# Kernel tuning notes

Hardware: AMD Instinct MI355X
Metric: run time of the kernel (lower is better)

The kernel has to match this reference:

```python
import jax, jax.numpy as jnp
import numpy as np

C, H, V, N, T = 256, 256, 10000, 8, 256


def _residual_mlp(x, w1, b1, w2, b2, w3, b3):
    # ResidualLayerOld: relu(lin2(relu(lin1(x)))) + x, then final Linear
    h = jax.nn.relu(x @ w1 + b1)
    h = jax.nn.relu(h @ w2 + b2) + x
    return h @ w3 + b3


def setup_inputs() -> dict:
    key = jax.random.key(0)
    ks = jax.random.split(key, 16)
    p = lambda k, shape: jax.random.normal(k, shape, jnp.float32) * 0.02
    return dict(
        text=jax.random.randint(ks[0], (N, T), 0, V),
        mask=jnp.ones((N, T), dtype=bool),
        lengths=jnp.full((N,), T - 1, dtype=jnp.int32),  # full-length sequences
        start_emb=jax.random.normal(ks[1], (C, H), jnp.float32),
        state_emb=jax.random.normal(ks[2], (C, H), jnp.float32),
        preterminal_emb=jax.random.normal(ks[3], (C, H), jnp.float32),
        start_w1=p(ks[4], (H, H)), start_b1=jnp.zeros((H,), jnp.float32),
        start_w2=p(ks[5], (H, H)), start_b2=jnp.zeros((H,), jnp.float32),
        start_w3=p(ks[6], (H, 1)), start_b3=jnp.zeros((1,), jnp.float32),
        trans_w1=p(ks[7], (H, H)), trans_b1=jnp.zeros((H,), jnp.float32),
        trans_w2=p(ks[8], (H, H)), trans_b2=jnp.zeros((H,), jnp.float32),
        trans_w3=p(ks[9], (H, C)), trans_b3=jnp.zeros((C,), jnp.float32),
        term_w1=p(ks[10], (H, H)), term_b1=jnp.zeros((H,), jnp.float32),
        term_w2=p(ks[11], (H, H)), term_b2=jnp.zeros((H,), jnp.float32),
        term_w3=p(ks[12], (H, V)), term_b3=jnp.zeros((V,), jnp.float32),
    )


def _score(text, mask, lengths,
           start_emb, state_emb, preterminal_emb,
           start_w1, start_b1, start_w2, start_b2, start_w3, start_b3,
           trans_w1, trans_b1, trans_w2, trans_b2, trans_w3, trans_b3,
           term_w1, term_b1, term_w2, term_b2, term_w3, term_b3):
    n, t = text.shape
    c = state_emb.shape[0]
    # start / transition / emission distributions (dropout_type == 'none')
    init = jax.nn.log_softmax(
        _residual_mlp(start_emb, start_w1, start_b1, start_w2, start_b2, start_w3, start_b3)[:, 0], -1)  # [C]
    trans = jax.nn.log_softmax(
        _residual_mlp(state_emb, trans_w1, trans_b1, trans_w2, trans_b2, trans_w3, trans_b3), -1)  # [C,C]
    log_em = jax.nn.log_softmax(
        _residual_mlp(preterminal_emb, term_w1, term_b1, term_w2, term_b2, term_w3, term_b3), -1)  # [C,V]
    obs = log_em.T[text]  # [N,T,C], log p(x_t | z=c)
    # torch_struct LinearChain.hmm edge potentials: phi[n,t,c_next,c_prev]
    phi = trans[None, None] + obs[:, 1:, :, None]  # [N,T-1,C,C]
    phi = phi.at[:, 0].add(init[None, None, :] + obs[:, 0][:, None, :])
    phi_t = jnp.swapaxes(phi, 0, 1)  # [T-1,N,C,C]

    def fwd_step(alpha, p):
        new = jax.nn.logsumexp(p + alpha[:, None, :], axis=-1)  # reduce over c_prev
        return new, new

    _, alphas = jax.lax.scan(fwd_step, jnp.zeros((n, c), phi.dtype), phi_t)  # [T-1,N,C]

    def bwd_step(beta, p):
        new = jax.nn.logsumexp(p + beta[:, :, None], axis=1)  # reduce over c_next
        return new, beta

    _, betas = jax.lax.scan(bwd_step, jnp.zeros((n, c), phi.dtype), phi_t, reverse=True)  # [T-1,N,C]

    alpha_prev = jnp.concatenate([jnp.zeros((1, n, c), phi.dtype), alphas[:-1]], 0)
    log_Z = jax.nn.logsumexp(alphas[-1], -1)  # [N]
    # edge posteriors
    log_m = alpha_prev[:, :, None, :] + phi_t + betas[:, :, :, None] - log_Z[None, :, None, None]
    marginals = jnp.swapaxes(jnp.exp(log_m), 0, 1)  # [N,T-1,C,C]

    evidence = jax.nn.logsumexp(alphas[lengths - 1, jnp.arange(n)], -1).sum()
    elbo = jnp.where(mask[:, 1:, None, None],
                     jax.lax.stop_gradient(marginals) * phi,
                     0.0).sum()
    return elbo, evidence


def reference(text, mask, lengths,
              start_emb, state_emb, preterminal_emb,
              start_w1, start_b1, start_w2, start_b2, start_w3, start_b3,
              trans_w1, trans_b1, trans_w2, trans_b2, trans_w3, trans_b3,
              term_w1, term_b1, term_w2, term_b2, term_w3, term_b3):
    elbo, evidence = _score(text, mask, lengths,
                            start_emb, state_emb, preterminal_emb,
                            start_w1, start_b1, start_w2, start_b2, start_w3, start_b3,
                            trans_w1, trans_b1, trans_w2, trans_b2, trans_w3, trans_b3,
                            term_w1, term_b1, term_w2, term_b2, term_w3, term_b3)
    return elbo, evidence
```

## Files before the change

kernel.cpp:

```cpp
#include <hip/hip_runtime.h>
#include <hip/hip_bf16.h>

#define C_ 256
#define H_ 256
#define V_ 10000
#define N_ 8
#define T_ 256
#define TM1_ 255
#define NB_ ((V_ + 31) / 32)

typedef _Float16 h2_t __attribute__((ext_vector_type(2)));
typedef _Float16 h4_t __attribute__((ext_vector_type(4)));
typedef _Float16 h8_t __attribute__((ext_vector_type(8)));
typedef float f4v __attribute__((ext_vector_type(4)));

__device__ __forceinline__ void bar_lgkm() {
  asm volatile("s_waitcnt lgkmcnt(0)\ns_barrier" ::: "memory");
}

__device__ __forceinline__ float wave_red_max(float v) {
#define DPP_MAX(ctrl) { int iv_ = __float_as_int(v); \
  int r_ = __builtin_amdgcn_update_dpp(iv_, iv_, ctrl, 0xF, 0xF, false); \
  v = fmaxf(v, __int_as_float(r_)); }
  DPP_MAX(0x111) DPP_MAX(0x112) DPP_MAX(0x114) DPP_MAX(0x118)
  DPP_MAX(0x142) DPP_MAX(0x143)
#undef DPP_MAX
  return __int_as_float(__builtin_amdgcn_readlane(__float_as_int(v), 63));
}
__device__ __forceinline__ float wave_red_sum(float v) {
#define DPP_ADD(ctrl) { \
  int r_ = __builtin_amdgcn_update_dpp(0, __float_as_int(v), ctrl, 0xF, 0xF, true); \
  v += __int_as_float(r_); }
  DPP_ADD(0x111) DPP_ADD(0x112) DPP_ADD(0x114) DPP_ADD(0x118)
  DPP_ADD(0x142) DPP_ADD(0x143)
#undef DPP_ADD
  return __int_as_float(__builtin_amdgcn_readlane(__float_as_int(v), 63));
}

__device__ __forceinline__ float block_allmax(float v, float* red) {
  v = wave_red_max(v);
  if ((threadIdx.x & 63) == 0) red[threadIdx.x >> 6] = v;
  __syncthreads();
  v = fmaxf(fmaxf(red[0], red[1]), fmaxf(red[2], red[3]));
  __syncthreads();
  return v;
}
__device__ __forceinline__ float block_allsum(float v, float* red) {
  v = wave_red_sum(v);
  if ((threadIdx.x & 63) == 0) red[threadIdx.x >> 6] = v;
  __syncthreads();
  v = (red[0] + red[1]) + (red[2] + red[3]);
  __syncthreads();
  return v;
}

__device__ __forceinline__ void mlp4(
    const float* __restrict__ emb,
    const float* __restrict__ w1, const float* __restrict__ b1,
    const float* __restrict__ w2, const float* __restrict__ b2,
    int r0, float (&e_s)[4][C_], float (&h_s)[4][C_], float (&h2_s)[4][C_]) {
  const int tid = threadIdx.x;
#pragma unroll
  for (int rr = 0; rr < 4; ++rr)
    e_s[rr][tid] = emb[(r0 + rr) * H_ + tid];
  __syncthreads();
  float bb = b1[tid];
  float a0 = bb, a1 = bb, a2 = bb, a3 = bb;
  for (int k4 = 0; k4 < H_ / 4; ++k4) {
    float4 e0 = ((const float4*)e_s[0])[k4];
    float4 e1 = ((const float4*)e_s[1])[k4];
    float4 e2 = ((const float4*)e_s[2])[k4];
    float4 e3 = ((const float4*)e_s[3])[k4];
    const float* wp = w1 + (k4 * 4) * H_ + tid;
    float wa = wp[0], wb = wp[H_], wc = wp[2 * H_], wd = wp[3 * H_];
    a0 = fmaf(e0.x, wa, a0); a0 = fmaf(e0.y, wb, a0);
    a0 = fmaf(e0.z, wc, a0); a0 = fmaf(e0.w, wd, a0);
    a1 = fmaf(e1.x, wa, a1); a1 = fmaf(e1.y, wb, a1);
    a1 = fmaf(e1.z, wc, a1); a1 = fmaf(e1.w, wd, a1);
    a2 = fmaf(e2.x, wa, a2); a2 = fmaf(e2.y, wb, a2);
    a2 = fmaf(e2.z, wc, a2); a2 = fmaf(e2.w, wd, a2);
    a3 = fmaf(e3.x, wa, a3); a3 = fmaf(e3.y, wb, a3);
    a3 = fmaf(e3.z, wc, a3); a3 = fmaf(e3.w, wd, a3);
  }
  h_s[0][tid] = fmaxf(a0, 0.f);
  h_s[1][tid] = fmaxf(a1, 0.f);
  h_s[2][tid] = fmaxf(a2, 0.f);
  h_s[3][tid] = fmaxf(a3, 0.f);
  __syncthreads();
  bb = b2[tid];
  a0 = bb; a1 = bb; a2 = bb; a3 = bb;
  for (int k4 = 0; k4 < H_ / 4; ++k4) {
    float4 e0 = ((const float4*)h_s[0])[k4];
    float4 e1 = ((const float4*)h_s[1])[k4];
    float4 e2 = ((const float4*)h_s[2])[k4];
    float4 e3 = ((const float4*)h_s[3])[k4];
    const float* wp = w2 + (k4 * 4) * H_ + tid;
    float wa = wp[0], wb = wp[H_], wc = wp[2 * H_], wd = wp[3 * H_];
    a0 = fmaf(e0.x, wa, a0); a0 = fmaf(e0.y, wb, a0);
    a0 = fmaf(e0.z, wc, a0); a0 = fmaf(e0.w, wd, a0);
    a1 = fmaf(e1.x, wa, a1); a1 = fmaf(e1.y, wb, a1);
    a1 = fmaf(e1.z, wc, a1); a1 = fmaf(e1.w, wd, a1);
    a2 = fmaf(e2.x, wa, a2); a2 = fmaf(e2.y, wb, a2);
    a2 = fmaf(e2.z, wc, a2); a2 = fmaf(e2.w, wd, a2);
    a3 = fmaf(e3.x, wa, a3); a3 = fmaf(e3.y, wb, a3);
    a3 = fmaf(e3.z, wc, a3); a3 = fmaf(e3.w, wd, a3);
  }
  h2_s[0][tid] = fmaxf(a0, 0.f) + e_s[0][tid];
  h2_s[1][tid] = fmaxf(a1, 0.f) + e_s[1][tid];
  h2_s[2][tid] = fmaxf(a2, 0.f) + e_s[2][tid];
  h2_s[3][tid] = fmaxf(a3, 0.f) + e_s[3][tid];
  __syncthreads();
}

__global__ __launch_bounds__(256) void k_start(
    const float* __restrict__ emb, const float* __restrict__ w1,
    const float* __restrict__ b1, const float* __restrict__ w2,
    const float* __restrict__ b2, const float* __restrict__ w3,
    const float* __restrict__ b3, float* __restrict__ slogit) {
  __shared__ __align__(16) float e_s[4][C_], h_s[4][C_], h2_s[4][C_];
  __shared__ float red[4];
  const int r0 = blockIdx.x * 4;
  const int tid = threadIdx.x;
  mlp4(emb, w1, b1, w2, b2, r0, e_s, h_s, h2_s);
  float w3v = w3[tid];
  float s0 = block_allsum(h2_s[0][tid] * w3v, red);
  float s1 = block_allsum(h2_s[1][tid] * w3v, red);
  float s2 = block_allsum(h2_s[2][tid] * w3v, red);
  float s3 = block_allsum(h2_s[3][tid] * w3v, red);
  if (tid == 0) {
    float bb = b3[0];
    slogit[r0 + 0] = s0 + bb;
    slogit[r0 + 1] = s1 + bb;
    slogit[r0 + 2] = s2 + bb;
    slogit[r0 + 3] = s3 + bb;
  }
}

__global__ void k_init(const float* __restrict__ slogit, float* __restrict__ initv) {
  __shared__ float red[4];
  const int tid = threadIdx.x;
  float x = slogit[tid];
  float m = block_allmax(x, red);
  float se = block_allsum(__expf(x - m), red);
  initv[tid] = x - m - __logf(se);
}

__global__ __launch_bounds__(256) void k_trans(
    const float* __restrict__ emb, const float* __restrict__ w1,
    const float* __restrict__ b1, const float* __restrict__ w2,
    const float* __restrict__ b2, const float* __restrict__ w3,
    const float* __restrict__ b3, float* __restrict__ Pf,
    float* __restrict__ PLf, float* __restrict__ PTf,
    _Float16* __restrict__ P_h, _Float16* __restrict__ PT_h) {
  __shared__ __align__(16) float e_s[4][C_], h_s[4][C_], h2_s[4][C_];
  __shared__ float red[4];
  const int r0 = blockIdx.x * 4;
  const int tid = threadIdx.x;
  mlp4(emb, w1, b1, w2, b2, r0, e_s, h_s, h2_s);
  float lb = b3[tid];
  float l0 = lb, l1 = lb, l2 = lb, l3 = lb;
  for (int k4 = 0; k4 < H_ / 4; ++k4) {
    float4 e0 = ((const float4*)h2_s[0])[k4];
    float4 e1 = ((const float4*)h2_s[1])[k4];
    float4 e2 = ((const float4*)h2_s[2])[k4];
    float4 e3 = ((const float4*)h2_s[3])[k4];
    const float* wp = w3 + (k4 * 4) * C_ + tid;
    float wa = wp[0], wb = wp[C_], wc = wp[2 * C_], wd = wp[3 * C_];
    l0 = fmaf(e0.x, wa, l0); l0 = fmaf(e0.y, wb, l0);
    l0 = fmaf(e0.z, wc, l0); l0 = fmaf(e0.w, wd, l0);
    l1 = fmaf(e1.x, wa, l1); l1 = fmaf(e1.y, wb, l1);
    l1 = fmaf(e1.z, wc, l1); l1 = fmaf(e1.w, wd, l1);
    l2 = fmaf(e2.x, wa, l2); l2 = fmaf(e2.y, wb, l2);
    l2 = fmaf(e2.z, wc, l2); l2 = fmaf(e2.w, wd, l2);
    l3 = fmaf(e3.x, wa, l3); l3 = fmaf(e3.y, wb, l3);
    l3 = fmaf(e3.z, wc, l3); l3 = fmaf(e3.w, wd, l3);
  }
  float lg[4] = {l0, l1, l2, l3};
#pragma unroll
  for (int rr = 0; rr < 4; ++rr) {
    float m = block_allmax(lg[rr], red);
    float e = __expf(lg[rr] - m);
    float se = block_allsum(e, red);
    float p = e / se;
    float tv = lg[rr] - m - __logf(se);
    const int r = r0 + rr;
    Pf[r * C_ + tid] = p;
    PLf[r * C_ + tid] = p * tv;
    PTf[tid * C_ + r] = p;
    P_h[r * C_ + tid] = (_Float16)p;
    PT_h[tid * C_ + r] = (_Float16)p;
  }
}

__global__ __launch_bounds__(256) void k_term_mlp(
    const float* __restrict__ emb, const float* __restrict__ w1,
    const float* __restrict__ b1, const float* __restrict__ w2,
    const float* __restrict__ b2, float* __restrict__ H2,
    float* __restrict__ H2T) {
  __shared__ __align__(16) float e_s[4][C_], h_s[4][C_], h2_s[4][C_];
  const int r0 = blockIdx.x * 4;
  const int tid = threadIdx.x;
  mlp4(emb, w1, b1, w2, b2, r0, e_s, h_s, h2_s);
#pragma unroll
  for (int rr = 0; rr < 4; ++rr) {
    const int r = r0 + rr;
    float v = h2_s[rr][tid];
    H2[r * H_ + tid] = v;
    H2T[tid * C_ + r] = v;
  }
}

__global__ __launch_bounds__(256) void k_term_stats(
    const float* __restrict__ H2, const float* __restrict__ w3,
    const float* __restrict__ b3, float* __restrict__ partm,
    float* __restrict__ parts) {
  __shared__ __align__(16) float w3_s[H_][32];
  __shared__ float b3_s[32];
  const int v0 = blockIdx.x * 32;
  const int tid = threadIdx.x;
  const int ncols = min(32, V_ - v0);
  for (int idx = tid; idx < H_ * 32; idx += 256) {
    int k = idx >> 5, c = idx & 31;
    w3_s[k][c] = (c < ncols) ? w3[k * V_ + v0 + c] : 0.f;
  }
  if (tid < 32) b3_s[tid] = (tid < ncols) ? b3[v0 + tid] : 0.f;
  __syncthreads();
  float acc[32];
#pragma unroll
  for (int c = 0; c < 32; ++c) acc[c] = 0.f;
  const float4* hq = (const float4*)(H2 + tid * H_);
  for (int k4 = 0; k4 < H_ / 4; ++k4) {
    float4 h = hq[k4];
    float hk[4];
    *(float4*)hk = h;
#pragma unroll
    for (int kk = 0; kk < 4; ++kk) {
      float hv = hk[kk];
      const int k = k4 * 4 + kk;
      const float4* wq = (const float4*)(&w3_s[k][0]);
#pragma unroll
      for (int c4 = 0; c4 < 8; ++c4) {
        float4 w = wq[c4];
        acc[c4 * 4 + 0] = fmaf(hv, w.x, acc[c4 * 4 + 0]);
        acc[c4 * 4 + 1] = fmaf(hv, w.y, acc[c4 * 4 + 1]);
        acc[c4 * 4 + 2] = fmaf(hv, w.z, acc[c4 * 4 + 2]);
        acc[c4 * 4 + 3] = fmaf(hv, w.w, acc[c4 * 4 + 3]);
      }
    }
  }
  float m = -1e30f;
#pragma unroll
  for (int c = 0; c < 32; ++c) {
    acc[c] += b3_s[c];
    if (c < ncols) m = fmaxf(m, acc[c]);
  }
  float se = 0.f;
#pragma unroll
  for (int c = 0; c < 32; ++c)
    if (c < ncols) se += __expf(acc[c] - m);
  partm[blockIdx.x * C_ + tid] = m;
  parts[blockIdx.x * C_ + tid] = se;
}

__global__ void k_denom(const float* __restrict__ partm,
                        const float* __restrict__ parts,
                        float* __restrict__ denom) {
  const int r = threadIdx.x;
  float m = -1e30f;
  for (int b = 0; b < NB_; ++b) m = fmaxf(m, partm[b * C_ + r]);
  float s = 0.f;
  for (int b = 0; b < NB_; ++b)
    s += parts[b * C_ + r] * __expf(partm[b * C_ + r] - m);
  denom[r] = m + __logf(s);
}

__global__ __launch_bounds__(256) void k_obs2(
    const int* __restrict__ text, const float* __restrict__ H2T,
    const float* __restrict__ w3, const float* __restrict__ b3,
    const float* __restrict__ denom, float* __restrict__ EOBS,
    float* __restrict__ Karr) {
  __shared__ __align__(16) float w_s[H_][8];
  __shared__ float redm[4][8];
  const int c = threadIdx.x;
  const int wid = c >> 6;
  const int lane = c & 63;
  const int base = blockIdx.x * 8;
  int tok[8];
#pragma unroll
  for (int i = 0; i < 8; ++i) tok[i] = text[base + i];
  float wtmp[8];
#pragma unroll
  for (int i = 0; i < 8; ++i) wtmp[i] = w3[c * V_ + tok[i]];
  float b3t[8];
#pragma unroll
  for (int i = 0; i < 8; ++i) b3t[i] = b3[tok[i]];
#pragma unroll
  for (int i = 0; i < 8; ++i) w_s[c][i] = wtmp[i];
  __syncthreads();
  float acc[8];
#pragma unroll
  for (int i = 0; i < 8; ++i) acc[i] = 0.f;
  for (int k4 = 0; k4 < H_ / 4; ++k4) {
    float hv[4];
#pragma unroll
    for (int kk = 0; kk < 4; ++kk) hv[kk] = H2T[(k4 * 4 + kk) * C_ + c];
#pragma unroll
    for (int kk = 0; kk < 4; ++kk) {
      const float4* wq = (const float4*)(&w_s[k4 * 4 + kk][0]);
      float4 wa = wq[0], wb = wq[1];
      acc[0] = fmaf(hv[kk], wa.x, acc[0]);
      acc[1] = fmaf(hv[kk], wa.y, acc[1]);
      acc[2] = fmaf(hv[kk], wa.z, acc[2]);
      acc[3] = fmaf(hv[kk], wa.w, acc[3]);
      acc[4] = fmaf(hv[kk], wb.x, acc[4]);
      acc[5] = fmaf(hv[kk], wb.y, acc[5]);
      acc[6] = fmaf(hv[kk], wb.z, acc[6]);
      acc[7] = fmaf(hv[kk], wb.w, acc[7]);
    }
  }
  float dn = denom[c];
  float obsv[8];
#pragma unroll
  for (int i = 0; i < 8; ++i) obsv[i] = acc[i] + b3t[i] - dn;
#pragma unroll
  for (int i = 0; i < 8; ++i) {
    float wm = wave_red_max(obsv[i]);
    if (lane == 0) redm[wid][i] = wm;
  }
  __syncthreads();
#pragma unroll
  for (int i = 0; i < 8; ++i) {
    float Ki = fmaxf(fmaxf(redm[0][i], redm[1][i]),
                     fmaxf(redm[2][i], redm[3][i]));
    EOBS[(base + i) * C_ + c] = __expf(obsv[i] - Ki);
    if (c == 0) Karr[base + i] = Ki;
  }
}

__global__ __launch_bounds__(256, 1) void k_scan4(
    const _Float16* __restrict__ P_h, const _Float16* __restrict__ PT_h,
    const float* __restrict__ initv, const float* __restrict__ EOBS,
    const float* __restrict__ Karr, float* __restrict__ AL,
    float* __restrict__ BL, float* __restrict__ CC, float* __restrict__ DD,
    float* __restrict__ LOGZ) {
  __shared__ __align__(16) _Float16 ubuf[2][C_];
  __shared__ float red[4];
  const int tid = threadIdx.x;
  const int wave = tid >> 6;
  const int lane = tid & 63;
  const int quad = lane >> 4;
  const int nn16 = lane & 15;
  const bool bwd = blockIdx.x >= N_;
  const int n = blockIdx.x & (N_ - 1);
  const _Float16* __restrict__ M = bwd ? PT_h : P_h;

  h8_t afrag[4][8];
#pragma unroll
  for (int mt = 0; mt < 4; ++mt) {
    const _Float16* rp = M + (size_t)((wave << 6) + (mt << 4) + nn16) * C_ + (quad << 3);
#pragma unroll
    for (int kt = 0; kt < 8; ++kt)
      afrag[mt][kt] = *(const h8_t*)(rp + (kt << 5));
  }
  const int stb = (wave << 6) + (quad << 2);

  if (!bwd) {
    float K0 = Karr[n * T_];
    f4v x0[4];
    float lmax = -1e30f;
#pragma unroll
    for (int mt = 0; mt < 4; ++mt) {
      const int st0 = stb + (mt << 4);
      f4v iv = *(const f4v*)(initv + st0);
      f4v e0 = *(const f4v*)(EOBS + (size_t)(n * T_) * C_ + st0);
#pragma unroll
      for (int r = 0; r < 4; ++r) {
        x0[mt][r] = iv[r] + __logf(e0[r]) + K0;
        lmax = fmaxf(lmax, x0[mt][r]);
      }
    }
    float wm = wave_red_max(lmax);
    if (lane == 0) red[wave] = wm;
    __syncthreads();
    float m0 = fmaxf(fmaxf(red[0], red[1]), fmaxf(red[2], red[3]));
    __syncthreads();
    float Cacc = m0;
    f4v uval[4];
#pragma unroll
    for (int mt = 0; mt < 4; ++mt) {
      const int st0 = stb + (mt << 4);
#pragma unroll
      for (int r = 0; r < 4; ++r) uval[mt][r] = __expf(x0[mt][r] - m0);
      if (nn16 == 0) {
        h4_t p;
#pragma unroll
        for (int r = 0; r < 4; ++r) p[r] = (_Float16)uval[mt][r];
        *(h4_t*)(&ubuf[0][st0]) = p;
        *(f4v*)(AL + (size_t)(0 * N_ + n) * C_ + st0) = uval[mt];
      }
    }
    if (tid == 0) CC[0 * N_ + n] = Cacc;
    float invm = 1.f, logm = 0.f;
    f4v eo_nx[4];
#pragma unroll
    for (int mt = 0; mt < 4; ++mt)
      eo_nx[mt] = *(const f4v*)(EOBS + (size_t)(n * T_ + 1) * C_ + stb + (mt << 4));
    float K_nx = Karr[n * T_ + 1];
    __syncthreads();

#pragma unroll 1
    for (int t = 0; t < TM1_; ++t) {
      const int cur = t & 1, nxt = cur ^ 1;
      f4v eo_pf[4];
      float K_pf = 0.f;
      if (t + 2 < T_) {
#pragma unroll
        for (int mt = 0; mt < 4; ++mt)
          eo_pf[mt] = *(const f4v*)(EOBS + (size_t)(n * T_ + t + 2) * C_ + stb + (mt << 4));
        K_pf = Karr[n * T_ + t + 2];
      }
      h8_t bf[8];
#pragma unroll
      for (int kt = 0; kt < 8; ++kt)
        bf[kt] = *(const h8_t*)(&ubuf[cur][(kt << 5) + (quad << 3)]);
      f4v acc[4];
#pragma unroll
      for (int mt = 0; mt < 4; ++mt) acc[mt] = (f4v){0.f, 0.f, 0.f, 0.f};
#pragma unroll
      for (int kt = 0; kt < 8; ++kt) {
#pragma unroll
        for (int mt = 0; mt < 4; ++mt)
          acc[mt] = __builtin_amdgcn_mfma_f32_16x16x32_f16(afrag[mt][kt], bf[kt], acc[mt], 0, 0, 0);
      }
      float lmx = -1e30f;
#pragma unroll
      for (int mt = 0; mt < 4; ++mt) {
#pragma unroll
        for (int r = 0; r < 4; ++r) {
          float u = acc[mt][r] * invm * eo_nx[mt][r];
          uval[mt][r] = u;
          lmx = fmaxf(lmx, u);
        }
      }
      Cacc += K_nx + logm;
      const bool resc = (t & 3) == 3;
      if (resc) {
        float wmm = wave_red_max(lmx);
        if (lane == 0) red[wave] = wmm;
      }
      if (nn16 == 0) {
#pragma unroll
        for (int mt = 0; mt < 4; ++mt) {
          const int st0 = stb + (mt << 4);
          h4_t p;
#pragma unroll
          for (int r = 0; r < 4; ++r) p[r] = (_Float16)uval[mt][r];
          *(h4_t*)(&ubuf[nxt][st0]) = p;
          *(f4v*)(AL + (size_t)((t + 1) * N_ + n) * C_ + st0) = uval[mt];
        }
      }
      if (tid == 0) CC[(t + 1) * N_ + n] = Cacc;
      bar_lgkm();
      if (resc) {
        float m = fmaxf(fmaxf(red[0], red[1]), fmaxf(red[2], red[3]));
        m = fmaxf(m, 1e-30f);
        invm = 1.f / m;
        logm = __logf(m);
      } else { invm = 1.f; logm = 0.f; }
#pragma unroll
      for (int mt = 0; mt < 4; ++mt) eo_nx[mt] = eo_pf[mt];
      K_nx = K_pf;
    }
    float s = 0.f;
#pragma unroll
    for (int mt = 0; mt < 4; ++mt)
      s += (uval[mt][0] + uval[mt][1]) + (uval[mt][2] + uval[mt][3]);
    s = wave_red_sum(s);
    if (lane == 0) red[wave] = s;
    __syncthreads();
    float S = ((red[0] + red[1]) + (red[2] + red[3])) * (1.f / 16.f);
    if (tid == 0) LOGZ[n] = __logf(S) + Cacc;
  } else {
    float Dacc = 0.f;
    f4v vval[4];
#pragma unroll
    for (int mt = 0; mt < 4; ++mt) {
      const int st0 = stb + (mt << 4);
      vval[mt] = *(const f4v*)(EOBS + ((size_t)n * T_ + TM1_) * C_ + st0);
      if (nn16 == 0) {
        h4_t p;
#pragma unroll
        for (int r = 0; r < 4; ++r) p[r] = (_Float16)vval[mt][r];
        *(h4_t*)(&ubuf[0][st0]) = p;
        f4v one = (f4v){1.f, 1.f, 1.f, 1.f};
        *(f4v*)(BL + (size_t)((TM1_ - 1) * N_ + n) * C_ + st0) = one;
      }
    }
    if (tid == 0) DD[(TM1_ - 1) * N_ + n] = 0.f;
    float K_nx = Karr[n * T_ + TM1_];
    f4v eo_nx[4];
#pragma unroll
    for (int mt = 0; mt < 4; ++mt)
      eo_nx[mt] = *(const f4v*)(EOBS + (size_t)(n * T_ + TM1_ - 1) * C_ + stb + (mt << 4));
    __syncthreads();

#pragma unroll 1
    for (int it = 0, t = TM1_ - 2; t >= 0; --t, ++it) {
      const int cur = it & 1, nxt = cur ^ 1;
      f4v eo_pf[4];
      float K_pf = 0.f;
      if (t >= 1) {
#pragma unroll
        for (int mt = 0; mt < 4; ++mt)
          eo_pf[mt] = *(const f4v*)(EOBS + (size_t)(n * T_ + t) * C_ + stb + (mt << 4));
        K_pf = Karr[n * T_ + t + 1];
      }
      float invm = 1.f, logm = 0.f;
      if ((it & 3) == 3) {
        float m = fmaxf(fmaxf(red[0], red[1]), fmaxf(red[2], red[3]));
        m = fmaxf(m, 1e-30f);
        invm = 1.f / m;
        logm = __logf(m);
      }
      h8_t bf[8];
#pragma unroll
      for (int kt = 0; kt < 8; ++kt)
        bf[kt] = *(const h8_t*)(&ubuf[cur][(kt << 5) + (quad << 3)]);
      f4v acc[4];
#pragma unroll
      for (int mt = 0; mt < 4; ++mt) acc[mt] = (f4v){0.f, 0.f, 0.f, 0.f};
#pragma unroll
      for (int kt = 0; kt < 8; ++kt) {
#pragma unroll
        for (int mt = 0; mt < 4; ++mt)
          acc[mt] = __builtin_amdgcn_mfma_f32_16x16x32_f16(afrag[mt][kt], bf[kt], acc[mt], 0, 0, 0);
      }
      Dacc += K_nx + logm;
      float lmx = -1e30f;
      f4v blv[4];
#pragma unroll
      for (int mt = 0; mt < 4; ++mt) {
#pragma unroll
        for (int r = 0; r < 4; ++r) {
          float b = acc[mt][r] * invm;
          blv[mt][r] = b;
          float v = b * eo_nx[mt][r];
          vval[mt][r] = v;
          lmx = fmaxf(lmx, v);
        }
      }
      if (((it + 1) & 3) == 3) {
        float wmm = wave_red_max(lmx);
        if (lane == 0) red[wave] = wmm;
      }
      if (nn16 == 0) {
#pragma unroll
        for (int mt = 0; mt < 4; ++mt) {
          const int st0 = stb + (mt << 4);
          h4_t p;
#pragma unroll
          for (int r = 0; r < 4; ++r) p[r] = (_Float16)vval[mt][r];
          *(h4_t*)(&ubuf[nxt][st0]) = p;
          *(f4v*)(BL + (size_t)(t * N_ + n) * C_ + st0) = blv[mt];
        }
      }
      if (tid == 0) DD[t * N_ + n] = Dacc;
      bar_lgkm();
#pragma unroll
      for (int mt = 0; mt < 4; ++mt) eo_nx[mt] = eo_pf[mt];
      K_nx = K_pf;
    }
  }
}

__global__ __launch_bounds__(256) void k_elbo(
    const float* __restrict__ Pf, const float* __restrict__ PLf,
    const float* __restrict__ PTf, const float* __restrict__ AL,
    const float* __restrict__ BL, const float* __restrict__ CC,
    const float* __restrict__ DD, const float* __restrict__ EOBS,
    const float* __restrict__ Karr, const float* __restrict__ LOGZ,
    float* __restrict__ out) {
  __shared__ __align__(16) float A_s[N_][C_];
  __shared__ __align__(16) float B_s[N_][C_];
  __shared__ float red[4];
  const int t = blockIdx.x;
  const int c = threadIdx.x;
  if (t == 0 && c == 0) {
    float s = 0.f;
#pragma unroll
    for (int nn = 0; nn < N_; ++nn) s += LOGZ[nn];
    out[1] = s;
  }
  float sc[N_], Kv[N_], cc[N_];
#pragma unroll
  for (int nn = 0; nn < N_; ++nn) {
    A_s[nn][c] = AL[(t * N_ + nn) * C_ + c];
    Kv[nn] = Karr[nn * T_ + t + 1];
    cc[nn] = CC[t * N_ + nn];
    sc[nn] = __expf(cc[nn] + DD[t * N_ + nn] + Kv[nn] - LOGZ[nn]);
  }
  __syncthreads();
  float accPA[N_], accPL[N_];
#pragma unroll
  for (int nn = 0; nn < N_; ++nn) { accPA[nn] = 0.f; accPL[nn] = 0.f; }
  const float4* pr = (const float4*)(Pf + c * C_);
  const float4* plr = (const float4*)(PLf + c * C_);
  for (int j = 0; j < C_ / 4; ++j) {
    float4 p = pr[j];
    float4 pl = plr[j];
#pragma unroll
    for (int nn = 0; nn < N_; ++nn) {
      float4 a = ((const float4*)A_s[nn])[j];
      accPA[nn] += p.x * a.x + p.y * a.y + p.z * a.z + p.w * a.w;
      accPL[nn] += pl.x * a.x + pl.y * a.y + pl.z * a.z + pl.w * a.w;
    }
  }
  float contrib = 0.f;
  float Bv[N_];
#pragma unroll
  for (int nn = 0; nn < N_; ++nn) {
    float eo = EOBS[(nn * T_ + t + 1) * C_ + c];
    float ob = __logf(eo) + Kv[nn];
    float B = eo * BL[(t * N_ + nn) * C_ + c] * sc[nn];
    Bv[nn] = B;
    contrib += B * fmaf(ob, accPA[nn], accPL[nn]);
  }
  if (t == 0) {
#pragma unroll
    for (int nn = 0; nn < N_; ++nn) B_s[nn][c] = Bv[nn];
    __syncthreads();
    const float4* ptq = (const float4*)(PTf + c * C_);
    float accPT[N_];
#pragma unroll
    for (int nn = 0; nn < N_; ++nn) accPT[nn] = 0.f;
    for (int j = 0; j < C_ / 4; ++j) {
      float4 p = ptq[j];
#pragma unroll
      for (int nn = 0; nn < N_; ++nn) {
        float4 b = ((const float4*)B_s[nn])[j];
        accPT[nn] += p.x * b.x + p.y * b.y + p.z * b.z + p.w * b.w;
      }
    }
#pragma unroll
    for (int nn = 0; nn < N_; ++nn) {
      float a0v = A_s[nn][c];
      if (a0v > 0.f)
        contrib += a0v * (__logf(a0v) + cc[nn]) * accPT[nn];
    }
  }
  contrib = wave_red_sum(contrib);
  if ((c & 63) == 0) red[c >> 6] = contrib;
  __syncthreads();
  if (c == 0) atomicAdd(out, (red[0] + red[1]) + (red[2] + red[3]));
}

extern "C" void kernel_launch(void* const* d_in, const int* in_sizes, int n_in,
                              void* d_out, int out_size, void* d_ws, size_t ws_size,
                              hipStream_t stream) {
  (void)in_sizes; (void)n_in; (void)out_size; (void)ws_size;
  const int* text = (const int*)d_in[0];
  const float* start_emb = (const float*)d_in[3];
  const float* state_emb = (const float*)d_in[4];
  const float* pre_emb   = (const float*)d_in[5];
  const float* sw1 = (const float*)d_in[6];  const float* sb1 = (const float*)d_in[7];
  const float* sw2 = (const float*)d_in[8];  const float* sb2 = (const float*)d_in[9];
  const float* sw3 = (const float*)d_in[10]; const float* sb3 = (const float*)d_in[11];
  const float* tw1 = (const float*)d_in[12]; const float* tb1 = (const float*)d_in[13];
  const float* tw2 = (const float*)d_in[14]; const float* tb2 = (const float*)d_in[15];
  const float* tw3 = (const float*)d_in[16]; const float* tb3 = (const float*)d_in[17];
  const float* ew1 = (const float*)d_in[18]; const float* eb1 = (const float*)d_in[19];
  const float* ew2 = (const float*)d_in[20]; const float* eb2 = (const float*)d_in[21];
  const float* ew3 = (const float*)d_in[22]; const float* eb3 = (const float*)d_in[23];
  float* out = (float*)d_out;

  char* p = (char*)d_ws;
  auto alloc = [&](size_t bytes) -> char* {
    char* r = p;
    p += (bytes + 255) & ~(size_t)255;
    return r;
  };
  float* slogit = (float*)alloc(C_ * 4);
  float* initv  = (float*)alloc(C_ * 4);
  float* denom  = (float*)alloc(C_ * 4);
  float* LOGZ   = (float*)alloc(N_ * 4);
  float* Pf     = (float*)alloc(C_ * C_ * 4);
  float* PLf    = (float*)alloc(C_ * C_ * 4);
  float* PTf    = (float*)alloc(C_ * C_ * 4);
  _Float16* P_h  = (_Float16*)alloc(C_ * C_ * 2);
  _Float16* PT_h = (_Float16*)alloc(C_ * C_ * 2);
  float* H2    = (float*)alloc(C_ * H_ * 4);
  float* H2T   = (float*)alloc(C_ * H_ * 4);
  float* partm = (float*)alloc(NB_ * C_ * 4);
  float* parts = (float*)alloc(NB_ * C_ * 4);
  float* EOBS  = (float*)alloc((size_t)N_ * T_ * C_ * 4);
  float* Karr  = (float*)alloc((size_t)N_ * T_ * 4);
  float* AL    = (float*)alloc((size_t)T_ * N_ * C_ * 4);
  float* BL    = (float*)alloc((size_t)TM1_ * N_ * C_ * 4);
  float* CC    = (float*)alloc((size_t)T_ * N_ * 4);
  float* DD    = (float*)alloc((size_t)TM1_ * N_ * 4);

  hipMemsetAsync(d_out, 0, 2 * sizeof(float), stream);

  k_start<<<dim3(C_ / 4), dim3(256), 0, stream>>>(start_emb, sw1, sb1, sw2, sb2, sw3, sb3, slogit);
  k_init<<<dim3(1), dim3(256), 0, stream>>>(slogit, initv);
  k_trans<<<dim3(C_ / 4), dim3(256), 0, stream>>>(state_emb, tw1, tb1, tw2, tb2, tw3, tb3,
                                                  Pf, PLf, PTf, P_h, PT_h);
  k_term_mlp<<<dim3(C_ / 4), dim3(256), 0, stream>>>(pre_emb, ew1, eb1, ew2, eb2, H2, H2T);
  k_term_stats<<<dim3(NB_), dim3(256), 0, stream>>>(H2, ew3, eb3, partm, parts);
  k_denom<<<dim3(1), dim3(256), 0, stream>>>(partm, parts, denom);
  k_obs2<<<dim3(N_ * T_ / 8), dim3(256), 0, stream>>>(text, H2T, ew3, eb3, denom, EOBS, Karr);
  k_scan4<<<dim3(2 * N_), dim3(256), 0, stream>>>(P_h, PT_h, initv, EOBS, Karr,
                                                  AL, BL, CC, DD, LOGZ);
  k_elbo<<<dim3(TM1_), dim3(256), 0, stream>>>(Pf, PLf, PTf, AL, BL, CC, DD,
                                               EOBS, Karr, LOGZ, out);
}
```

Measured before the change: 551.5 us.

## Transpose emission weights, deepen scan prefetch, move stores after barrier, split elbo grid

A new kernel transposes the emission output weights so the observation kernel gathers contiguous rows per token instead of strided columns. The scan kernel now prefetches emission data two steps ahead and issues the alpha/beta global stores after the barrier, taking them off the critical path. The ELBO kernel's grid is split over two halves of the batch for more parallelism, and the denominator loops are unrolled. The extra transpose kernel reads and writes the full 10 MB weight matrix on every call, which may cost more than the gather it replaces.

```diff
diff --git a/kernel.cpp b/kernel.cpp
--- a/kernel.cpp
+++ b/kernel.cpp
@@ -8,6 +8,7 @@
 #define T_ 256
 #define TM1_ 255
 #define NB_ ((V_ + 31) / 32)
+#define VT_ ((V_ + 31) / 32)
 
 typedef _Float16 h2_t __attribute__((ext_vector_type(2)));
 typedef _Float16 h4_t __attribute__((ext_vector_type(4)));
@@ -52,6 +53,27 @@
   v = (red[0] + red[1]) + (red[2] + red[3]);
   __syncthreads();
   return v;
+}
+
+__global__ __launch_bounds__(256) void k_w3t(const float* __restrict__ w3,
+                                             float* __restrict__ w3T) {
+  __shared__ float t_s[32][33];
+  const int tx = threadIdx.x & 31;
+  const int ty = threadIdx.x >> 5;
+  const int v0 = blockIdx.x * 32;
+  const int k0 = blockIdx.y * 32;
+#pragma unroll
+  for (int r = 0; r < 4; ++r) {
+    int k = k0 + ty + r * 8;
+    int v = v0 + tx;
+    if (v < V_) t_s[ty + r * 8][tx] = w3[k * V_ + v];
+  }
+  __syncthreads();
+#pragma unroll
+  for (int r = 0; r < 4; ++r) {
+    int v = v0 + ty + r * 8;
+    if (v < V_) w3T[(size_t)v * H_ + k0 + tx] = t_s[tx][ty + r * 8];
+  }
 }
 
 __device__ __forceinline__ void mlp4(
@@ -267,16 +289,18 @@
                         float* __restrict__ denom) {
   const int r = threadIdx.x;
   float m = -1e30f;
+#pragma unroll 8
   for (int b = 0; b < NB_; ++b) m = fmaxf(m, partm[b * C_ + r]);
   float s = 0.f;
+#pragma unroll 8
   for (int b = 0; b < NB_; ++b)
     s += parts[b * C_ + r] * __expf(partm[b * C_ + r] - m);
   denom[r] = m + __logf(s);
 }
 
-__global__ __launch_bounds__(256) void k_obs2(
+__global__ __launch_bounds__(256) void k_obs3(
     const int* __restrict__ text, const float* __restrict__ H2T,
-    const float* __restrict__ w3, const float* __restrict__ b3,
+    const float* __restrict__ w3T, const float* __restrict__ b3,
     const float* __restrict__ denom, float* __restrict__ EOBS,
     float* __restrict__ Karr) {
   __shared__ __align__(16) float w_s[H_][8];
@@ -290,7 +314,7 @@
   for (int i = 0; i < 8; ++i) tok[i] = text[base + i];
   float wtmp[8];
 #pragma unroll
-  for (int i = 0; i < 8; ++i) wtmp[i] = w3[c * V_ + tok[i]];
+  for (int i = 0; i < 8; ++i) wtmp[i] = w3T[(size_t)tok[i] * H_ + c];
   float b3t[8];
 #pragma unroll
   for (int i = 0; i < 8; ++i) b3t[i] = b3[tok[i]];
@@ -337,7 +361,7 @@
   }
 }
 
-__global__ __launch_bounds__(256, 1) void k_scan4(
+__global__ __launch_bounds__(256, 1) void k_scan5(
     const _Float16* __restrict__ P_h, const _Float16* __restrict__ PT_h,
     const float* __restrict__ initv, const float* __restrict__ EOBS,
     const float* __restrict__ Karr, float* __restrict__ AL,
@@ -401,23 +425,25 @@
     }
     if (tid == 0) CC[0 * N_ + n] = Cacc;
     float invm = 1.f, logm = 0.f;
-    f4v eo_nx[4];
-#pragma unroll
-    for (int mt = 0; mt < 4; ++mt)
-      eo_nx[mt] = *(const f4v*)(EOBS + (size_t)(n * T_ + 1) * C_ + stb + (mt << 4));
-    float K_nx = Karr[n * T_ + 1];
+    f4v eoA[4], eoB[4];
+#pragma unroll
+    for (int mt = 0; mt < 4; ++mt) {
+      eoA[mt] = *(const f4v*)(EOBS + (size_t)(n * T_ + 1) * C_ + stb + (mt << 4));
+      eoB[mt] = *(const f4v*)(EOBS + (size_t)(n * T_ + 2) * C_ + stb + (mt << 4));
+    }
+    float KA = Karr[n * T_ + 1], KB = Karr[n * T_ + 2];
     __syncthreads();
 
 #pragma unroll 1
     for (int t = 0; t < TM1_; ++t) {
       const int cur = t & 1, nxt = cur ^ 1;
-      f4v eo_pf[4];
-      float K_pf = 0.f;
-      if (t + 2 < T_) {
+      f4v eoC[4];
+      float KC = 0.f;
+      if (t + 3 < T_) {
 #pragma unroll
         for (int mt = 0; mt < 4; ++mt)
-          eo_pf[mt] = *(const f4v*)(EOBS + (size_t)(n * T_ + t + 2) * C_ + stb + (mt << 4));
-        K_pf = Karr[n * T_ + t + 2];
+          eoC[mt] = *(const f4v*)(EOBS + (size_t)(n * T_ + t + 3) * C_ + stb + (mt << 4));
+        KC = Karr[n * T_ + t + 3];
       }
       h8_t bf[8];
 #pragma unroll
@@ -437,12 +463,12 @@
       for (int mt = 0; mt < 4; ++mt) {
 #pragma unroll
         for (int r = 0; r < 4; ++r) {
-          float u = acc[mt][r] * invm * eo_nx[mt][r];
+          float u = acc[mt][r] * invm * eoA[mt][r];
           uval[mt][r] = u;
           lmx = fmaxf(lmx, u);
         }
       }
-      Cacc += K_nx + logm;
+      Cacc += KA + logm;
       const bool resc = (t & 3) == 3;
       if (resc) {
         float wmm = wave_red_max(lmx);
@@ -456,11 +482,15 @@
 #pragma unroll
           for (int r = 0; r < 4; ++r) p[r] = (_Float16)uval[mt][r];
           *(h4_t*)(&ubuf[nxt][st0]) = p;
-          *(f4v*)(AL + (size_t)((t + 1) * N_ + n) * C_ + st0) = uval[mt];
         }
       }
+      bar_lgkm();
+      if (nn16 == 0) {
+#pragma unroll
+        for (int mt = 0; mt < 4; ++mt)
+          *(f4v*)(AL + (size_t)((t + 1) * N_ + n) * C_ + stb + (mt << 4)) = uval[mt];
+      }
       if (tid == 0) CC[(t + 1) * N_ + n] = Cacc;
-      bar_lgkm();
       if (resc) {
         float m = fmaxf(fmaxf(red[0], red[1]), fmaxf(red[2], red[3]));
         m = fmaxf(m, 1e-30f);
@@ -468,8 +498,8 @@
         logm = __logf(m);
       } else { invm = 1.f; logm = 0.f; }
 #pragma unroll
-      for (int mt = 0; mt < 4; ++mt) eo_nx[mt] = eo_pf[mt];
-      K_nx = K_pf;
+      for (int mt = 0; mt < 4; ++mt) { eoA[mt] = eoB[mt]; eoB[mt] = eoC[mt]; }
+      KA = KB; KB = KC;
     }
     float s = 0.f;
 #pragma unroll
@@ -497,23 +527,25 @@
       }
     }
     if (tid == 0) DD[(TM1_ - 1) * N_ + n] = 0.f;
-    float K_nx = Karr[n * T_ + TM1_];
-    f4v eo_nx[4];
-#pragma unroll
-    for (int mt = 0; mt < 4; ++mt)
-      eo_nx[mt] = *(const f4v*)(EOBS + (size_t)(n * T_ + TM1_ - 1) * C_ + stb + (mt << 4));
+    f4v eoA[4], eoB[4];
+#pragma unroll
+    for (int mt = 0; mt < 4; ++mt) {
+      eoA[mt] = *(const f4v*)(EOBS + (size_t)(n * T_ + TM1_ - 1) * C_ + stb + (mt << 4));
+      eoB[mt] = *(const f4v*)(EOBS + (size_t)(n * T_ + TM1_ - 2) * C_ + stb + (mt << 4));
+    }
+    float KA = Karr[n * T_ + TM1_], KB = Karr[n * T_ + TM1_ - 1];
     __syncthreads();
 
 #pragma unroll 1
     for (int it = 0, t = TM1_ - 2; t >= 0; --t, ++it) {
       const int cur = it & 1, nxt = cur ^ 1;
-      f4v eo_pf[4];
-      float K_pf = 0.f;
-      if (t >= 1) {
+      f4v eoC[4];
+      float KC = 0.f;
+      if (t >= 2) {
 #pragma unroll
         for (int mt = 0; mt < 4; ++mt)
-          eo_pf[mt] = *(const f4v*)(EOBS + (size_t)(n * T_ + t) * C_ + stb + (mt << 4));
-        K_pf = Karr[n * T_ + t + 1];
+          eoC[mt] = *(const f4v*)(EOBS + (size_t)(n * T_ + t - 1) * C_ + stb + (mt << 4));
+        KC = Karr[n * T_ + t];
       }
       float invm = 1.f, logm = 0.f;
       if ((it & 3) == 3) {
@@ -535,7 +567,7 @@
         for (int mt = 0; mt < 4; ++mt)
           acc[mt] = __builtin_amdgcn_mfma_f32_16x16x32_f16(afrag[mt][kt], bf[kt], acc[mt], 0, 0, 0);
       }
-      Dacc += K_nx + logm;
+      Dacc += KA + logm;
       float lmx = -1e30f;
       f4v blv[4];
 #pragma unroll
@@ -544,7 +576,7 @@
         for (int r = 0; r < 4; ++r) {
           float b = acc[mt][r] * invm;
           blv[mt][r] = b;
-          float v = b * eo_nx[mt][r];
+          float v = b * eoA[mt][r];
           vval[mt][r] = v;
           lmx = fmaxf(lmx, v);
         }
@@ -561,18 +593,23 @@
 #pragma unroll
           for (int r = 0; r < 4; ++r) p[r] = (_Float16)vval[mt][r];
           *(h4_t*)(&ubuf[nxt][st0]) = p;
-          *(f4v*)(BL + (size_t)(t * N_ + n) * C_ + st0) = blv[mt];
         }
       }
+      bar_lgkm();
+      if (nn16 == 0) {
+#pragma unroll
+        for (int mt = 0; mt < 4; ++mt)
+          *(f4v*)(BL + (size_t)(t * N_ + n) * C_ + stb + (mt << 4)) = blv[mt];
+      }
       if (tid == 0) DD[t * N_ + n] = Dacc;
-      bar_lgkm();
-#pragma unroll
-      for (int mt = 0; mt < 4; ++mt) eo_nx[mt] = eo_pf[mt];
-      K_nx = K_pf;
-    }
-  }
-}
-
+#pragma unroll
+      for (int mt = 0; mt < 4; ++mt) { eoA[mt] = eoB[mt]; eoB[mt] = eoC[mt]; }
+      KA = KB; KB = KC;
+    }
+  }
+}
+
+#define NH_ 4
 __global__ __launch_bounds__(256) void k_elbo(
     const float* __restrict__ Pf, const float* __restrict__ PLf,
     const float* __restrict__ PTf, const float* __restrict__ AL,
@@ -580,69 +617,72 @@
     const float* __restrict__ DD, const float* __restrict__ EOBS,
     const float* __restrict__ Karr, const float* __restrict__ LOGZ,
     float* __restrict__ out) {
-  __shared__ __align__(16) float A_s[N_][C_];
-  __shared__ __align__(16) float B_s[N_][C_];
+  __shared__ __align__(16) float A_s[NH_][C_];
+  __shared__ __align__(16) float B_s[NH_][C_];
   __shared__ float red[4];
   const int t = blockIdx.x;
+  const int nb = blockIdx.y * NH_;
   const int c = threadIdx.x;
-  if (t == 0 && c == 0) {
+  if (t == 0 && blockIdx.y == 0 && c == 0) {
     float s = 0.f;
 #pragma unroll
     for (int nn = 0; nn < N_; ++nn) s += LOGZ[nn];
     out[1] = s;
   }
-  float sc[N_], Kv[N_], cc[N_];
-#pragma unroll
-  for (int nn = 0; nn < N_; ++nn) {
-    A_s[nn][c] = AL[(t * N_ + nn) * C_ + c];
-    Kv[nn] = Karr[nn * T_ + t + 1];
-    cc[nn] = CC[t * N_ + nn];
-    sc[nn] = __expf(cc[nn] + DD[t * N_ + nn] + Kv[nn] - LOGZ[nn]);
-  }
-  __syncthreads();
-  float accPA[N_], accPL[N_];
-#pragma unroll
-  for (int nn = 0; nn < N_; ++nn) { accPA[nn] = 0.f; accPL[nn] = 0.f; }
+  float sc[NH_], Kv[NH_], cc[NH_];
+#pragma unroll
+  for (int nn = 0; nn < NH_; ++nn) {
+    const int n = nb + nn;
+    A_s[nn][c] = AL[(t * N_ + n) * C_ + c];
+    Kv[nn] = Karr[n * T_ + t + 1];
+    cc[nn] = CC[t * N_ + n];
+    sc[nn] = __expf(cc[nn] + DD[t * N_ + n] + Kv[nn] - LOGZ[n]);
+  }
+  __syncthreads();
+  float accPA[NH_], accPL[NH_];
+#pragma unroll
+  for (int nn = 0; nn < NH_; ++nn) { accPA[nn] = 0.f; accPL[nn] = 0.f; }
   const float4* pr = (const float4*)(Pf + c * C_);
   const float4* plr = (const float4*)(PLf + c * C_);
   for (int j = 0; j < C_ / 4; ++j) {
     float4 p = pr[j];
     float4 pl = plr[j];
 #pragma unroll
-    for (int nn = 0; nn < N_; ++nn) {
+    for (int nn = 0; nn < NH_; ++nn) {
       float4 a = ((const float4*)A_s[nn])[j];
       accPA[nn] += p.x * a.x + p.y * a.y + p.z * a.z + p.w * a.w;
       accPL[nn] += pl.x * a.x + pl.y * a.y + pl.z * a.z + pl.w * a.w;
     }
   }
   float contrib = 0.f;
-  float Bv[N_];
-#pragma unroll
-  for (int nn = 0; nn < N_; ++nn) {
-    float eo = EOBS[(nn * T_ + t + 1) * C_ + c];
+  float Bv[NH_];
+#pragma unroll
+  for (int nn = 0; nn < NH_; ++nn) {
+    const int n = nb + nn;
+    float eo = EOBS[(n * T_ + t + 1) * C_ + c];
     float ob = __logf(eo) + Kv[nn];
-    float B = eo * BL[(t * N_ + nn) * C_ + c] * sc[nn];
+    float B = eo * BL[(t * N_ + n) * C_ + c] * sc[nn];
     Bv[nn] = B;
     contrib += B * fmaf(ob, accPA[nn], accPL[nn]);
   }
   if (t == 0) {
 #pragma unroll
-    for (int nn = 0; nn < N_; ++nn) B_s[nn][c] = Bv[nn];
+    for (int nn = 0; nn < NH_; ++nn) B_s[nn][c] = Bv[nn];
     __syncthreads();
     const float4* ptq = (const float4*)(PTf + c * C_);
-    float accPT[N_];
-#pragma unroll
-    for (int nn = 0; nn < N_; ++nn) accPT[nn] = 0.f;
+    float accPT[NH_];
+#pragma unroll
+    for (int nn = 0; nn < NH_; ++nn) accPT[nn] = 0.f;
     for (int j = 0; j < C_ / 4; ++j) {
       float4 p = ptq[j];
 #pragma unroll
-      for (int nn = 0; nn < N_; ++nn) {
+      for (int nn = 0; nn < NH_; ++nn) {
         float4 b = ((const float4*)B_s[nn])[j];
         accPT[nn] += p.x * b.x + p.y * b.y + p.z * b.z + p.w * b.w;
       }
     }
 #pragma unroll
-    for (int nn = 0; nn < N_; ++nn) {
+    for (int nn = 0; nn < NH_; ++nn) {
       float a0v = A_s[nn][c];
       if (a0v > 0.f)
         contrib += a0v * (__logf(a0v) + cc[nn]) * accPT[nn];
@@ -692,6 +732,7 @@
   float* H2T   = (float*)alloc(C_ * H_ * 4);
   float* partm = (float*)alloc(NB_ * C_ * 4);
   float* parts = (float*)alloc(NB_ * C_ * 4);
+  float* w3T   = (float*)alloc((size_t)V_ * H_ * 4);
   float* EOBS  = (float*)alloc((size_t)N_ * T_ * C_ * 4);
   float* Karr  = (float*)alloc((size_t)N_ * T_ * 4);
   float* AL    = (float*)alloc((size_t)T_ * N_ * C_ * 4);
@@ -701,6 +742,7 @@
 
   hipMemsetAsync(d_out, 0, 2 * sizeof(float), stream);
 
+  k_w3t<<<dim3(VT_, H_ / 32), dim3(256), 0, stream>>>(ew3, w3T);
   k_start<<<dim3(C_ / 4), dim3(256), 0, stream>>>(start_emb, sw1, sb1, sw2, sb2, sw3, sb3, slogit);
   k_init<<<dim3(1), dim3(256), 0, stream>>>(slogit, initv);
   k_trans<<<dim3(C_ / 4), dim3(256), 0, stream>>>(state_emb, tw1, tb1, tw2, tb2, tw3, tb3,
@@ -708,9 +750,9 @@
   k_term_mlp<<<dim3(C_ / 4), dim3(256), 0, stream>>>(pre_emb, ew1, eb1, ew2, eb2, H2, H2T);
   k_term_stats<<<dim3(NB_), dim3(256), 0, stream>>>(H2, ew3, eb3, partm, parts);
   k_denom<<<dim3(1), dim3(256), 0, stream>>>(partm, parts, denom);
-  k_obs2<<<dim3(N_ * T_ / 8), dim3(256), 0, stream>>>(text, H2T, ew3, eb3, denom, EOBS, Karr);
-  k_scan4<<<dim3(2 * N_), dim3(256), 0, stream>>>(P_h, PT_h, initv, EOBS, Karr,
+  k_obs3<<<dim3(N_ * T_ / 8), dim3(256), 0, stream>>>(text, H2T, w3T, eb3, denom, EOBS, Karr);
+  k_scan5<<<dim3(2 * N_), dim3(256), 0, stream>>>(P_h, PT_h, initv, EOBS, Karr,
                                                   AL, BL, CC, DD, LOGZ);
-  k_elbo<<<dim3(TM1_), dim3(256), 0, stream>>>(Pf, PLf, PTf, AL, BL, CC, DD,
-                                               EOBS, Karr, LOGZ, out);
-}
+  k_elbo<<<dim3(TM1_, 2), dim3(256), 0, stream>>>(Pf, PLf, PTf, AL, BL, CC, DD,
+                                                  EOBS, Karr, LOGZ, out);
+}
```

Measured after the change: 596.5 us. 1.08x slower.
